# Optimization experiments

Hardware: AMD Instinct MI355X
Metric: run time of the kernel (lower is better)

## Reference

```python
import jax, jax.numpy as jnp
import numpy as np

TOKENS, D_IN = 8192, 1024
E, D_OUT = 8, 1024
H = 2 * D_OUT  # Expert hidden = 2 * num_outputs


def setup_inputs() -> dict:
    key = jax.random.key(0)
    ks = jax.random.split(key, 4)
    s_in = 1.0 / np.sqrt(D_IN)
    s_h = 1.0 / np.sqrt(H)
    return {
        "x": jax.random.normal(ks[0], (TOKENS, D_IN), dtype=jnp.float32),
        "W1": jax.random.normal(ks[1], (E, D_IN, H), dtype=jnp.float32) * s_in,
        "b1": jnp.zeros((E, H), dtype=jnp.float32),
        "W2": jax.random.normal(ks[2], (E, H, D_OUT), dtype=jnp.float32) * s_h,
        "b2": jnp.zeros((E, D_OUT), dtype=jnp.float32),
        "Wg": jax.random.normal(ks[3], (D_IN, E), dtype=jnp.float32) * s_in,
        "bg": jnp.zeros((E,), dtype=jnp.float32),
    }


def reference(x, W1, b1, W2, b2, Wg, bg):
    # Gating: softmax over experts. gates: [N, E]
    gates = jax.nn.softmax(x @ Wg + bg, axis=-1)
    # All experts run densely: batched GEMM over expert axis.
    h = jax.nn.relu(jnp.einsum('nd,edh->neh', x, W1) + b1)       # [N, E, H]
    expert_out = jnp.einsum('neh,ehf->nef', h, W2) + b2          # [N, E, D_OUT]
    # Gate-weighted sum over experts (fused stack*gate->sum).
    return jnp.einsum('nef,ne->nf', expert_out, gates)            # [N, D_OUT]
```

## Files before the change

kernel.cpp:

```cpp
#include <hip/hip_runtime.h>
#include <stdint.h>

#define TOKENS 8192
#define D_IN   1024
#define NEXP   8
#define D_OUT  1024
#define HDIM   2048

typedef __bf16 bf16x8 __attribute__((ext_vector_type(8)));
typedef __bf16 bf16x4 __attribute__((ext_vector_type(4)));
typedef float  f32x4  __attribute__((ext_vector_type(4)));

__device__ __forceinline__ void gload16(const void* g, void* l) {
  __builtin_amdgcn_global_load_lds(
      (const __attribute__((address_space(1))) void*)g,
      (__attribute__((address_space(3))) void*)l,
      16, 0, 0);
}

__global__ void gate_kernel(const float* __restrict__ x,
                            const float* __restrict__ Wg,
                            const float* __restrict__ bg,
                            float* __restrict__ gates) {
  const int lane = threadIdx.x & 63;
  const int n = blockIdx.x * 4 + (threadIdx.x >> 6);
  float acc[NEXP];
#pragma unroll
  for (int e = 0; e < NEXP; ++e) acc[e] = 0.f;
  const float* xr = x + (size_t)n * D_IN;
  for (int d = lane; d < D_IN; d += 64) {
    float xv = xr[d];
    const float* wr = Wg + d * NEXP;
#pragma unroll
    for (int e = 0; e < NEXP; ++e) acc[e] += xv * wr[e];
  }
#pragma unroll
  for (int e = 0; e < NEXP; ++e) {
    float v = acc[e];
#pragma unroll
    for (int off = 32; off > 0; off >>= 1) v += __shfl_down(v, off);
    acc[e] = v;
  }
  if (lane == 0) {
    float mx = -1e30f;
#pragma unroll
    for (int e = 0; e < NEXP; ++e) { acc[e] += bg[e]; mx = fmaxf(mx, acc[e]); }
    float s = 0.f;
#pragma unroll
    for (int e = 0; e < NEXP; ++e) { acc[e] = expf(acc[e] - mx); s += acc[e]; }
    float inv = 1.f / s;
#pragma unroll
    for (int e = 0; e < NEXP; ++e) gates[n * NEXP + e] = acc[e] * inv;
  }
}

__global__ void cvt_x_kernel(const float* __restrict__ x, __bf16* __restrict__ xb) {
  const int stride = gridDim.x * blockDim.x;
  const int total4 = TOKENS * D_IN / 4;
  for (int i = blockIdx.x * blockDim.x + threadIdx.x; i < total4; i += stride) {
    float4 v = ((const float4*)x)[i];
    bf16x4 o;
    o[0] = (__bf16)v.x; o[1] = (__bf16)v.y; o[2] = (__bf16)v.z; o[3] = (__bf16)v.w;
    ((bf16x4*)xb)[i] = o;
  }
}

__global__ void transpose_cvt_kernel(const float* __restrict__ W,
                                     __bf16* __restrict__ Wt,
                                     int K, int N) {
  __shared__ float tile[32][33];
  const int e = blockIdx.z;
  const float* Win = W + (size_t)e * K * N;
  __bf16* Wout = Wt + (size_t)e * K * N;
  const int n0 = blockIdx.x * 32;
  const int k0 = blockIdx.y * 32;
  const int tx = threadIdx.x & 31;
  const int ty = threadIdx.x >> 5;
#pragma unroll
  for (int r = ty; r < 32; r += 8)
    tile[r][tx] = Win[(size_t)(k0 + r) * N + n0 + tx];
  __syncthreads();
#pragma unroll
  for (int r = ty; r < 32; r += 8)
    Wout[(size_t)(n0 + r) * K + k0 + tx] = (__bf16)tile[tx][r];
}

template <int BN, int WM, int WN, int EPI>
__global__ __launch_bounds__(512, 2)
void gemm_bt_kernel(const __bf16* __restrict__ A,
                    const __bf16* __restrict__ B,
                    const float* __restrict__ bias,
                    const float* __restrict__ gates,
                    int e, int first,
                    __bf16* __restrict__ Hout,
                    float* __restrict__ Fout,
                    int M, int N, int K) {
  constexpr int BM = 256;
  constexpr int ABYTES = BM * 64 * 2;
  constexpr int BBYTES = BN * 64 * 2;
  constexpr int SLOT   = (ABYTES + BBYTES) / 2;
  constexpr int LOADS  = (ABYTES + BBYTES) / (512 * 16);
  constexpr int FM = (BM / WM) / 16;
  constexpr int FN = (BN / WN) / 16;
  __shared__ alignas(16) __bf16 lds[2 * SLOT];

  const int tid  = threadIdx.x;
  const int lane = tid & 63;
  const int wave = tid >> 6;
  const int wr   = wave / WN;
  const int wc   = wave % WN;
  const int lrow = lane & 15;
  const int khi  = lane >> 4;

  const int Gx   = gridDim.x;
  const int nwg  = Gx * gridDim.y;
  const int orig = blockIdx.y * Gx + blockIdx.x;
  const int wgid = (orig & 7) * (nwg >> 3) + (orig >> 3);
  const int bn0  = (wgid % Gx) * BN;
  const int bm0  = (wgid / Gx) * BM;

  const __bf16* gsrc[LOADS];
#pragma unroll
  for (int i = 0; i < LOADS; ++i) {
    int o    = i * 8192 + tid * 16;
    bool isA = (o < ABYTES);
    int oo   = isA ? o : (o - ABYTES);
    int row  = oo >> 7;
    int scb  = (oo & 127) ^ ((row & 7) << 4);
    const __bf16* base =
        isA ? (A + (size_t)(bm0 + row) * K) : (B + (size_t)(bn0 + row) * K);
    gsrc[i] = base + (scb >> 1);
  }

  f32x4 acc[FM][FN];
#pragma unroll
  for (int m = 0; m < FM; ++m)
#pragma unroll
    for (int n = 0; n < FN; ++n) acc[m][n] = f32x4{0.f, 0.f, 0.f, 0.f};

  const int arow0 = wr * (BM / WM) + lrow;
  const int brow0 = wc * (BN / WN) + lrow;
  const int sx    = (lrow & 7) << 3;

  auto stage = [&](int kt, int s) {
#pragma unroll
    for (int i = 0; i < LOADS; ++i)
      gload16(gsrc[i] + kt * 64, lds + s * SLOT + i * 4096 + wave * 512);
  };

  const int nk = K / 64;
  stage(0, 0);
  for (int t = 0; t < nk; ++t) {
    const int s = t & 1;
    if (t + 1 < nk) {
      stage(t + 1, s ^ 1);
      if constexpr (LOADS == 8) asm volatile("s_waitcnt vmcnt(8)" ::: "memory");
      else                      asm volatile("s_waitcnt vmcnt(6)" ::: "memory");
    } else {
      asm volatile("s_waitcnt vmcnt(0)" ::: "memory");
    }
    asm volatile("s_barrier" ::: "memory");

    const __bf16* As = lds + s * SLOT;
    const __bf16* Bs = As + ABYTES / 2;
#pragma unroll
    for (int kk = 0; kk < 2; ++kk) {
      const int c = (kk * 32 + khi * 8) ^ sx;
      bf16x8 af[FM], bfv[FN];
#pragma unroll
      for (int m = 0; m < FM; ++m)
        af[m] = *(const bf16x8*)&As[(arow0 + m * 16) * 64 + c];
#pragma unroll
      for (int n = 0; n < FN; ++n)
        bfv[n] = *(const bf16x8*)&Bs[(brow0 + n * 16) * 64 + c];
      __builtin_amdgcn_s_setprio(1);
#pragma unroll
      for (int m = 0; m < FM; ++m)
#pragma unroll
        for (int n = 0; n < FN; ++n)
          acc[m][n] = __builtin_amdgcn_mfma_f32_16x16x32_bf16(af[m], bfv[n], acc[m][n], 0, 0, 0);
      __builtin_amdgcn_s_setprio(0);
    }
    asm volatile("s_barrier" ::: "memory");
  }

#pragma unroll
  for (int m = 0; m < FM; ++m) {
    const int grow0 = bm0 + wr * (BM / WM) + m * 16 + khi * 4;
    float g[4];
    if constexpr (EPI == 1) {
#pragma unroll
      for (int r = 0; r < 4; ++r) g[r] = gates[(size_t)(grow0 + r) * NEXP + e];
    }
#pragma unroll
    for (int n = 0; n < FN; ++n) {
      const int gcol = bn0 + wc * (BN / WN) + n * 16 + lrow;
      const float bv = bias[gcol];
      f32x4 a = acc[m][n];
      if constexpr (EPI == 0) {
#pragma unroll
        for (int r = 0; r < 4; ++r) {
          float v = a[r] + bv;
          v = v > 0.f ? v : 0.f;
          Hout[(size_t)(grow0 + r) * N + gcol] = (__bf16)v;
        }
      } else {
#pragma unroll
        for (int r = 0; r < 4; ++r) {
          float v = (a[r] + bv) * g[r];
          float* o = Fout + (size_t)(grow0 + r) * N + gcol;
          if (first) *o = v;
          else       *o += v;
        }
      }
    }
  }
}

extern "C" void kernel_launch(void* const* d_in, const int* in_sizes, int n_in,
                              void* d_out, int out_size, void* d_ws, size_t ws_size,
                              hipStream_t stream) {
  const float* x  = (const float*)d_in[0];
  const float* W1 = (const float*)d_in[1];
  const float* b1 = (const float*)d_in[2];
  const float* W2 = (const float*)d_in[3];
  const float* b2 = (const float*)d_in[4];
  const float* Wg = (const float*)d_in[5];
  const float* bg = (const float*)d_in[6];
  float* out = (float*)d_out;

  char* w = (char*)d_ws;
  float* gates = (float*)w;            w += (size_t)TOKENS * NEXP * 4;
  __bf16* xb   = (__bf16*)w;           w += (size_t)TOKENS * D_IN * 2;
  __bf16* w1t  = (__bf16*)w;           w += (size_t)NEXP * HDIM * D_IN * 2;
  __bf16* w2t  = (__bf16*)w;           w += (size_t)NEXP * D_OUT * HDIM * 2;
  __bf16* hbuf = (__bf16*)w;

  gate_kernel<<<TOKENS / 4, 256, 0, stream>>>(x, Wg, bg, gates);
  cvt_x_kernel<<<2048, 256, 0, stream>>>(x, xb);
  transpose_cvt_kernel<<<dim3(HDIM / 32, D_IN / 32, NEXP), 256, 0, stream>>>(W1, w1t, D_IN, HDIM);
  transpose_cvt_kernel<<<dim3(D_OUT / 32, HDIM / 32, NEXP), 256, 0, stream>>>(W2, w2t, HDIM, D_OUT);

  for (int e = 0; e < NEXP; ++e) {
    const __bf16* w1e = w1t + (size_t)e * HDIM * D_IN;
    const __bf16* w2e = w2t + (size_t)e * D_OUT * HDIM;
    gemm_bt_kernel<256, 2, 4, 0><<<dim3(HDIM / 256, TOKENS / 256), 512, 0, stream>>>(
        xb, w1e, b1 + (size_t)e * HDIM, nullptr, e, 0,
        hbuf, nullptr, TOKENS, HDIM, D_IN);
    gemm_bt_kernel<128, 4, 2, 1><<<dim3(D_OUT / 128, TOKENS / 256), 512, 0, stream>>>(
        hbuf, w2e, b2 + (size_t)e * D_OUT, gates, e, (e == 0) ? 1 : 0,
        nullptr, out, TOKENS, D_OUT, HDIM);
  }
}
```

Measured before the change: 794.5 us.

## Split GEMM K-tile into quadrant clusters interleaving LDS reads, prefetch and MFMA

The GEMM main loop is restructured so each 256xBN tile is processed as four quadrant clusters. Each quadrant's LDS fragment reads and the next tile's global-to-LDS prefetch of the matching A/B half are interleaved with the MFMA work of the preceding quadrant. The goal is to hide global-load and LDS latency behind matrix-core work instead of doing one bulk wait per K step. In exchange each iteration carries more barriers, and fragments must be held for both B halves, which raises register pressure.

```diff
diff --git a/kernel.cpp b/kernel.cpp
--- a/kernel.cpp
+++ b/kernel.cpp
@@ -16,6 +16,16 @@
       (const __attribute__((address_space(1))) void*)g,
       (__attribute__((address_space(3))) void*)l,
       16, 0, 0);
+}
+
+template <int N>
+__device__ __forceinline__ void waitv() {
+  if constexpr (N == 0)      asm volatile("s_waitcnt vmcnt(0)" ::: "memory");
+  else if constexpr (N == 1) asm volatile("s_waitcnt vmcnt(1)" ::: "memory");
+  else if constexpr (N == 2) asm volatile("s_waitcnt vmcnt(2)" ::: "memory");
+  else if constexpr (N == 3) asm volatile("s_waitcnt vmcnt(3)" ::: "memory");
+  else if constexpr (N == 4) asm volatile("s_waitcnt vmcnt(4)" ::: "memory");
+  else static_assert(N <= 4, "unsupported vmcnt");
 }
 
 __global__ void gate_kernel(const float* __restrict__ x,
@@ -85,23 +95,22 @@
     Wout[(size_t)(n0 + r) * K + k0 + tx] = (__bf16)tile[tx][r];
 }
 
-template <int BN, int WM, int WN, int EPI>
+template <int BM, int BN, int WM, int WN, int EPI>
 __global__ __launch_bounds__(512, 2)
-void gemm_bt_kernel(const __bf16* __restrict__ A,
-                    const __bf16* __restrict__ B,
-                    const float* __restrict__ bias,
-                    const float* __restrict__ gates,
-                    int e, int first,
-                    __bf16* __restrict__ Hout,
-                    float* __restrict__ Fout,
-                    int M, int N, int K) {
-  constexpr int BM = 256;
-  constexpr int ABYTES = BM * 64 * 2;
-  constexpr int BBYTES = BN * 64 * 2;
-  constexpr int SLOT   = (ABYTES + BBYTES) / 2;
-  constexpr int LOADS  = (ABYTES + BBYTES) / (512 * 16);
-  constexpr int FM = (BM / WM) / 16;
-  constexpr int FN = (BN / WN) / 16;
+void gemm_q4(const __bf16* __restrict__ A,
+             const __bf16* __restrict__ Bbase, size_t Bstride_e,
+             const float* __restrict__ biasbase, int bias_stride_e,
+             const float* __restrict__ gates,
+             int e, int first,
+             __bf16* __restrict__ Hout, float* __restrict__ Fout,
+             int M, int N, int K, int ldo) {
+  constexpr int RM = BM / WM, RN = BN / WN;
+  constexpr int FM = RM / 16, FN = RN / 16;
+  constexpr int HM = FM / 2,  HN = FN / 2;
+  constexpr int LA = BM / 128;
+  constexpr int LB = BN / 128;
+  constexpr int AELEM = BM * 64;
+  constexpr int SLOT  = (BM + BN) * 64;
   __shared__ alignas(16) __bf16 lds[2 * SLOT];
 
   const int tid  = threadIdx.x;
@@ -111,6 +120,10 @@
   const int wc   = wave % WN;
   const int lrow = lane & 15;
   const int khi  = lane >> 4;
+  const int sx   = (lrow & 7) << 3;
+
+  const __bf16* Bp   = Bbase + (size_t)e * Bstride_e;
+  const float*  bias = biasbase + (size_t)e * bias_stride_e;
 
   const int Gx   = gridDim.x;
   const int nwg  = Gx * gridDim.y;
@@ -119,18 +132,38 @@
   const int bn0  = (wgid % Gx) * BN;
   const int bm0  = (wgid / Gx) * BM;
 
-  const __bf16* gsrc[LOADS];
-#pragma unroll
-  for (int i = 0; i < LOADS; ++i) {
-    int o    = i * 8192 + tid * 16;
-    bool isA = (o < ABYTES);
-    int oo   = isA ? o : (o - ABYTES);
-    int row  = oo >> 7;
-    int scb  = (oo & 127) ^ ((row & 7) << 4);
-    const __bf16* base =
-        isA ? (A + (size_t)(bm0 + row) * K) : (B + (size_t)(bn0 + row) * K);
-    gsrc[i] = base + (scb >> 1);
-  }
+  const __bf16* srcA[2][LA];
+  const __bf16* srcB[2][LB];
+#pragma unroll
+  for (int q = 0; q < 2; ++q) {
+#pragma unroll
+    for (int j = 0; j < LA; ++j) {
+      int o   = q * (BM * 64) + j * 8192 + tid * 16;
+      int row = o >> 7;
+      int cb  = (o & 127) ^ ((row & 7) << 4);
+      srcA[q][j] = A + (size_t)(bm0 + row) * K + (cb >> 1);
+    }
+#pragma unroll
+    for (int j = 0; j < LB; ++j) {
+      int o   = q * (BN * 64) + j * 8192 + tid * 16;
+      int row = o >> 7;
+      int cb  = (o & 127) ^ ((row & 7) << 4);
+      srcB[q][j] = Bp + (size_t)(bn0 + row) * K + (cb >> 1);
+    }
+  }
+
+  auto stageA = [&](int kt, int q, int s) {
+#pragma unroll
+    for (int j = 0; j < LA; ++j)
+      gload16(srcA[q][j] + (size_t)kt * 64,
+              lds + s * SLOT + q * (BM * 32) + j * 4096 + wave * 512);
+  };
+  auto stageB = [&](int kt, int q, int s) {
+#pragma unroll
+    for (int j = 0; j < LB; ++j)
+      gload16(srcB[q][j] + (size_t)kt * 64,
+              lds + s * SLOT + AELEM + q * (BN * 32) + j * 4096 + wave * 512);
+  };
 
   f32x4 acc[FM][FN];
 #pragma unroll
@@ -138,77 +171,116 @@
 #pragma unroll
     for (int n = 0; n < FN; ++n) acc[m][n] = f32x4{0.f, 0.f, 0.f, 0.f};
 
-  const int arow0 = wr * (BM / WM) + lrow;
-  const int brow0 = wc * (BN / WN) + lrow;
-  const int sx    = (lrow & 7) << 3;
-
-  auto stage = [&](int kt, int s) {
-#pragma unroll
-    for (int i = 0; i < LOADS; ++i)
-      gload16(gsrc[i] + kt * 64, lds + s * SLOT + i * 4096 + wave * 512);
-  };
-
-  const int nk = K / 64;
-  stage(0, 0);
+  bf16x8 af[HM][2];
+  bf16x8 bf[2][HN][2];
+
+  auto rdA = [&](const __bf16* As, int mq) {
+#pragma unroll
+    for (int mi = 0; mi < HM; ++mi)
+#pragma unroll
+      for (int kk = 0; kk < 2; ++kk)
+        af[mi][kk] = *(const bf16x8*)
+            &As[(size_t)(mq * (BM / 2) + wr * (RM / 2) + mi * 16 + lrow) * 64 +
+                ((kk * 32 + khi * 8) ^ sx)];
+  };
+  auto rdB = [&](const __bf16* Bs, int nq) {
+#pragma unroll
+    for (int ni = 0; ni < HN; ++ni)
+#pragma unroll
+      for (int kk = 0; kk < 2; ++kk)
+        bf[nq][ni][kk] = *(const bf16x8*)
+            &Bs[(size_t)(nq * (BN / 2) + wc * (RN / 2) + ni * 16 + lrow) * 64 +
+                ((kk * 32 + khi * 8) ^ sx)];
+  };
+  auto cluster = [&](int mq, int nq) {
+    __builtin_amdgcn_s_setprio(1);
+#pragma unroll
+    for (int kk = 0; kk < 2; ++kk)
+#pragma unroll
+      for (int mi = 0; mi < HM; ++mi)
+#pragma unroll
+        for (int ni = 0; ni < HN; ++ni)
+          acc[mq * HM + mi][nq * HN + ni] =
+              __builtin_amdgcn_mfma_f32_16x16x32_bf16(
+                  af[mi][kk], bf[nq][ni][kk], acc[mq * HM + mi][nq * HN + ni],
+                  0, 0, 0);
+    __builtin_amdgcn_s_setprio(0);
+  };
+
+#define BAR()   asm volatile("s_barrier" ::: "memory")
+#define LGKM0() do { asm volatile("s_waitcnt lgkmcnt(0)" ::: "memory"); \
+                     __builtin_amdgcn_sched_barrier(0); } while (0)
+
+  const int nk = K >> 6;
+
+  stageA(0, 0, 0); stageB(0, 0, 0); stageA(0, 1, 0); stageB(0, 1, 0);
+  waitv<0>();
+  BAR();
+
   for (int t = 0; t < nk; ++t) {
     const int s = t & 1;
-    if (t + 1 < nk) {
-      stage(t + 1, s ^ 1);
-      if constexpr (LOADS == 8) asm volatile("s_waitcnt vmcnt(8)" ::: "memory");
-      else                      asm volatile("s_waitcnt vmcnt(6)" ::: "memory");
-    } else {
-      asm volatile("s_waitcnt vmcnt(0)" ::: "memory");
-    }
-    asm volatile("s_barrier" ::: "memory");
-
     const __bf16* As = lds + s * SLOT;
-    const __bf16* Bs = As + ABYTES / 2;
-#pragma unroll
-    for (int kk = 0; kk < 2; ++kk) {
-      const int c = (kk * 32 + khi * 8) ^ sx;
-      bf16x8 af[FM], bfv[FN];
-#pragma unroll
-      for (int m = 0; m < FM; ++m)
-        af[m] = *(const bf16x8*)&As[(arow0 + m * 16) * 64 + c];
-#pragma unroll
-      for (int n = 0; n < FN; ++n)
-        bfv[n] = *(const bf16x8*)&Bs[(brow0 + n * 16) * 64 + c];
-      __builtin_amdgcn_s_setprio(1);
-#pragma unroll
-      for (int m = 0; m < FM; ++m)
-#pragma unroll
-        for (int n = 0; n < FN; ++n)
-          acc[m][n] = __builtin_amdgcn_mfma_f32_16x16x32_bf16(af[m], bfv[n], acc[m][n], 0, 0, 0);
-      __builtin_amdgcn_s_setprio(0);
-    }
-    asm volatile("s_barrier" ::: "memory");
-  }
+    const __bf16* Bs = As + AELEM;
+    const bool pf = (t + 1 < nk);
+
+    rdA(As, 0); rdB(Bs, 0);
+    if (pf) stageA(t + 1, 0, s ^ 1);
+    BAR(); LGKM0();
+    cluster(0, 0);
+    if (pf) waitv<LA>(); else waitv<0>();
+    BAR();
+    rdB(Bs, 1);
+    if (pf) stageB(t + 1, 0, s ^ 1);
+    BAR(); LGKM0();
+    cluster(0, 1);
+    BAR();
+    rdA(As, 1);
+    if (pf) stageA(t + 1, 1, s ^ 1);
+    BAR(); LGKM0();
+    cluster(1, 0);
+    BAR();
+    if (pf) stageB(t + 1, 1, s ^ 1);
+    BAR();
+    cluster(1, 1);
+    if (pf) waitv<LA + LB>(); else waitv<0>();
+    BAR();
+  }
+
+#undef BAR
+#undef LGKM0
 
 #pragma unroll
   for (int m = 0; m < FM; ++m) {
-    const int grow0 = bm0 + wr * (BM / WM) + m * 16 + khi * 4;
-    float g[4];
-    if constexpr (EPI == 1) {
-#pragma unroll
-      for (int r = 0; r < 4; ++r) g[r] = gates[(size_t)(grow0 + r) * NEXP + e];
-    }
-#pragma unroll
-    for (int n = 0; n < FN; ++n) {
-      const int gcol = bn0 + wc * (BN / WN) + n * 16 + lrow;
-      const float bv = bias[gcol];
-      f32x4 a = acc[m][n];
-      if constexpr (EPI == 0) {
+    const int grow0 = bm0 + (m / HM) * (BM / 2) + wr * (RM / 2) +
+                      (m % HM) * 16 + khi * 4;
+    if constexpr (EPI == 0) {
+#pragma unroll
+      for (int n = 0; n < FN; ++n) {
+        const int gcol = bn0 + (n / HN) * (BN / 2) + wc * (RN / 2) +
+                         (n % HN) * 16 + lrow;
+        const float bv = bias[gcol];
+        f32x4 a = acc[m][n];
 #pragma unroll
         for (int r = 0; r < 4; ++r) {
           float v = a[r] + bv;
           v = v > 0.f ? v : 0.f;
-          Hout[(size_t)(grow0 + r) * N + gcol] = (__bf16)v;
+          Hout[(size_t)(grow0 + r) * ldo + gcol] = (__bf16)v;
         }
-      } else {
+      }
+    } else {
+      float g[4];
+#pragma unroll
+      for (int r = 0; r < 4; ++r) g[r] = gates[(size_t)(grow0 + r) * NEXP + e];
+#pragma unroll
+      for (int n = 0; n < FN; ++n) {
+        const int gcol = bn0 + (n / HN) * (BN / 2) + wc * (RN / 2) +
+                         (n % HN) * 16 + lrow;
+        const float bv = bias[gcol];
+        f32x4 a = acc[m][n];
 #pragma unroll
         for (int r = 0; r < 4; ++r) {
           float v = (a[r] + bv) * g[r];
-          float* o = Fout + (size_t)(grow0 + r) * N + gcol;
+          float* o = Fout + (size_t)(grow0 + r) * ldo + gcol;
           if (first) *o = v;
           else       *o += v;
         }
@@ -230,25 +302,25 @@
   float* out = (float*)d_out;
 
   char* w = (char*)d_ws;
-  float* gates = (float*)w;            w += (size_t)TOKENS * NEXP * 4;
-  __bf16* xb   = (__bf16*)w;           w += (size_t)TOKENS * D_IN * 2;
-  __bf16* w1t  = (__bf16*)w;           w += (size_t)NEXP * HDIM * D_IN * 2;
-  __bf16* w2t  = (__bf16*)w;           w += (size_t)NEXP * D_OUT * HDIM * 2;
+  float* gates = (float*)w;   w += (size_t)TOKENS * NEXP * 4;
+  __bf16* xb   = (__bf16*)w;  w += (size_t)TOKENS * D_IN * 2;
+  __bf16* w1t  = (__bf16*)w;  w += (size_t)NEXP * HDIM * D_IN * 2;
+  __bf16* w2t  = (__bf16*)w;  w += (size_t)NEXP * D_OUT * HDIM * 2;
   __bf16* hbuf = (__bf16*)w;
 
   gate_kernel<<<TOKENS / 4, 256, 0, stream>>>(x, Wg, bg, gates);
   cvt_x_kernel<<<2048, 256, 0, stream>>>(x, xb);
-  transpose_cvt_kernel<<<dim3(HDIM / 32, D_IN / 32, NEXP), 256, 0, stream>>>(W1, w1t, D_IN, HDIM);
-  transpose_cvt_kernel<<<dim3(D_OUT / 32, HDIM / 32, NEXP), 256, 0, stream>>>(W2, w2t, HDIM, D_OUT);
+  transpose_cvt_kernel<<<dim3(HDIM / 32, D_IN / 32, NEXP), 256, 0, stream>>>(
+      W1, w1t, D_IN, HDIM);
+  transpose_cvt_kernel<<<dim3(D_OUT / 32, HDIM / 32, NEXP), 256, 0, stream>>>(
+      W2, w2t, HDIM, D_OUT);
 
   for (int e = 0; e < NEXP; ++e) {
-    const __bf16* w1e = w1t + (size_t)e * HDIM * D_IN;
-    const __bf16* w2e = w2t + (size_t)e * D_OUT * HDIM;
-    gemm_bt_kernel<256, 2, 4, 0><<<dim3(HDIM / 256, TOKENS / 256), 512, 0, stream>>>(
-        xb, w1e, b1 + (size_t)e * HDIM, nullptr, e, 0,
-        hbuf, nullptr, TOKENS, HDIM, D_IN);
-    gemm_bt_kernel<128, 4, 2, 1><<<dim3(D_OUT / 128, TOKENS / 256), 512, 0, stream>>>(
-        hbuf, w2e, b2 + (size_t)e * D_OUT, gates, e, (e == 0) ? 1 : 0,
-        nullptr, out, TOKENS, D_OUT, HDIM);
-  }
-}
+    gemm_q4<256, 256, 2, 4, 0><<<dim3(HDIM / 256, TOKENS / 256), 512, 0, stream>>>(
+        xb, w1t, (size_t)HDIM * D_IN, b1, HDIM, gates,
+        e, 0, hbuf, nullptr, TOKENS, HDIM, D_IN, HDIM);
+    gemm_q4<256, 128, 4, 2, 1><<<dim3(D_OUT / 128, TOKENS / 256), 512, 0, stream>>>(
+        hbuf, w2t, (size_t)D_OUT * HDIM, b2, D_OUT, gates,
+        e, (e == 0) ? 1 : 0, nullptr, out, TOKENS, D_OUT, HDIM, D_OUT);
+  }
+}
```

New measurement: 811.1 us. 2.1% more time.
